# Optimization experiments

Hardware: AMD Instinct MI355X
Metric: run time of the kernel (lower is better)

## Reference

```python
import jax, jax.numpy as jnp
import numpy as np
from jax import lax

ALPHA = 0.1
B, C_IN, T, D_MODEL = 32, 512, 2048, 1024


def setup_inputs() -> dict:
    key = jax.random.key(0)
    k_x, k_w, k_b = jax.random.split(key, 3)
    x = jax.random.normal(k_x, (B, C_IN, T), dtype=jnp.float32)
    # nn.Linear(c_in, d_model): weight [d_model, c_in], bias [d_model]
    bound = 1.0 / np.sqrt(C_IN)
    W = jax.random.uniform(k_w, (D_MODEL, C_IN), dtype=jnp.float32, minval=-bound, maxval=bound)
    b = jax.random.uniform(k_b, (D_MODEL,), dtype=jnp.float32, minval=-bound, maxval=bound)
    return {"x": x, "W": W, "b": b}


def _ewma_scan(xt):
    # xt: [T, B, C] time-major; f_0 = x_0, f_t = a*x_t + (1-a)*f_{t-1}
    def step(carry, xi):
        carry = ALPHA * xi + (1.0 - ALPHA) * carry
        return carry, carry
    _, ys = lax.scan(step, xt[0], xt[1:])
    return jnp.concatenate([xt[:1], ys], axis=0)  # [T, B, C]


def reference(x, W, b):
    # x: [B, c_in, T] -> permute to [B, T, c_in]
    xp = jnp.transpose(x, (0, 2, 1))
    xt = jnp.moveaxis(xp, 1, 0)  # [T, B, c_in]
    fwd = _ewma_scan(xt)
    bwd = _ewma_scan(xt[::-1])[::-1]
    ewma = jnp.moveaxis((fwd + bwd) * 0.5, 0, 1)  # [B, T, c_in]
    # value embedding (dropout = identity at inference)
    return jnp.einsum('btc,dc->btd', ewma, W) + b
```

## Files before the change

kernel.cpp:

```cpp
#include <hip/hip_runtime.h>
#include <hip/hip_bf16.h>
#include <stdint.h>
#include <stddef.h>

#define T_LEN   2048
#define C_IN_   512
#define D_MODEL_ 1024
#define B_SZ    32

typedef __hip_bfloat16 bf16;
typedef __attribute__((ext_vector_type(8))) short short8;
typedef __attribute__((ext_vector_type(4))) float f32x4;

__device__ __forceinline__ void gload16(const void* g, void* l) {
    __builtin_amdgcn_global_load_lds(
        (const __attribute__((address_space(1))) uint32_t*)g,
        (__attribute__((address_space(3))) uint32_t*)l, 16, 0, 0);
}

__global__ void wconv_kernel(const float* __restrict__ W, bf16* __restrict__ Wb) {
    int i = blockIdx.x * 256 + threadIdx.x;
    float4 v = ((const float4*)W)[i];
    bf16* o = Wb + (size_t)i * 4;
    o[0] = __float2bfloat16(v.x);
    o[1] = __float2bfloat16(v.y);
    o[2] = __float2bfloat16(v.z);
    o[3] = __float2bfloat16(v.w);
}

__global__ __launch_bounds__(512)
void ewma_kernel(const float* __restrict__ x, bf16* __restrict__ A) {
    const int tid  = threadIdx.x;
    const int wid  = tid >> 6;
    const int lane = tid & 63;
    const int half = lane >> 5;
    const int j    = lane & 31;
    const int b    = blockIdx.x >> 5;
    const int cg   = blockIdx.x & 31;
    const int c_local = (wid << 1) | half;

    const float AL = 0.1f, OM = 0.9f;
    const float Q  = 1.179018457773862e-3f;

    __shared__ float buf[8 * 2048];
    __shared__ bf16  stg[32 * 16 * 16];

    float xr[64];
    const size_t xbase = ((size_t)b * C_IN_ + (cg << 4)) * T_LEN;
    const int srcu = tid ^ ((tid >> 4) & 7);

    #pragma unroll
    for (int h = 0; h < 2; ++h) {
        #pragma unroll
        for (int it = 0; it < 8; ++it)
            gload16(x + xbase + (size_t)(h * 8 + it) * T_LEN + srcu * 4,
                    (char*)buf + it * 8192 + tid * 16);
        asm volatile("s_waitcnt vmcnt(0)" ::: "memory");
        __syncthreads();
        if ((c_local >> 3) == h) {
            const char* rbase = (const char*)buf + (c_local & 7) * 8192;
            #pragma unroll
            for (int i = 0; i < 16; ++i) {
                int p = (j * 16 + i) ^ (j & 7);
                float4 v = *(const float4*)(rbase + p * 16);
                xr[4*i+0] = v.x; xr[4*i+1] = v.y;
                xr[4*i+2] = v.z; xr[4*i+3] = v.w;
            }
        }
        __syncthreads();
    }

    float g = (j == 0) ? xr[0] : AL * xr[0];
    #pragma unroll
    for (int i = 1; i < 64; ++i) g = fmaf(OM, g, AL * xr[i]);

    float F = g, coef = Q;
    #pragma unroll
    for (int d = 1; d < 32; d <<= 1) {
        float up = __shfl_up(F, d, 32);
        F += (j >= d) ? coef * up : 0.0f;
        coef *= coef;
    }
    float carry = __shfl_up(F, 1, 32);
    if (j == 0) carry = 0.0f;

    xr[0] = (j == 0) ? xr[0] : fmaf(OM, carry, AL * xr[0]);
    #pragma unroll
    for (int i = 1; i < 64; ++i) xr[i] = fmaf(OM, xr[i-1], AL * xr[i]);

    float h2;
    {
        float incL = xr[63] - OM * xr[62];
        if (j == 31) incL *= 10.0f;
        h2 = incL;
        #pragma unroll
        for (int i = 62; i >= 1; --i) h2 = fmaf(OM, h2, xr[i] - OM * xr[i-1]);
        float inc0 = (j == 0) ? AL * xr[0] : (xr[0] - OM * carry);
        h2 = fmaf(OM, h2, inc0);
    }

    float Bv = h2; coef = Q;
    #pragma unroll
    for (int d = 1; d < 32; d <<= 1) {
        float dn = __shfl_down(Bv, d, 32);
        Bv += (j < 32 - d) ? coef * dn : 0.0f;
        coef *= coef;
    }
    float bnext = __shfl_down(Bv, 1, 32);
    if (j == 31) bnext = 0.0f;

    {
        float bp = bnext;
        float incL = xr[63] - OM * xr[62];
        if (j == 31) incL *= 10.0f;
        float bb = fmaf(OM, bp, incL);
        xr[63] = 0.5f * (xr[63] + bb);
        bp = bb;
        #pragma unroll
        for (int i = 62; i >= 1; --i) {
            float inc = xr[i] - OM * xr[i-1];
            bb = fmaf(OM, bp, inc);
            xr[i] = 0.5f * (xr[i] + bb);
            bp = bb;
        }
        float inc0 = (j == 0) ? AL * xr[0] : (xr[0] - OM * carry);
        bb = fmaf(OM, bp, inc0);
        xr[0] = 0.5f * (xr[0] + bb);
    }

    const size_t outbase = (size_t)(b * T_LEN) * C_IN_ + (cg << 4);
    #pragma unroll
    for (int grp = 0; grp < 4; ++grp) {
        __syncthreads();
        #pragma unroll
        for (int ii = 0; ii < 16; ++ii) {
            int elem = ((j * 16 + ii) * 16 + c_local) ^ ((j & 7) << 3);
            stg[elem] = __float2bfloat16(xr[grp * 16 + ii]);
        }
        __syncthreads();
        #pragma unroll
        for (int r = 0; r < 2; ++r) {
            int u   = tid * 2 + r;
            int jj  = u >> 5;
            int ii  = (u >> 1) & 15;
            int hf  = u & 1;
            int elem = ((jj * 16 + ii) * 16 + hf * 8) ^ ((jj & 7) << 3);
            float4 v = *(const float4*)&stg[elem];
            int t = jj * 64 + grp * 16 + ii;
            *(float4*)(A + outbase + (size_t)t * C_IN_ + hf * 8) = v;
        }
    }
}

#define MFMA(a, b, c) __builtin_amdgcn_mfma_f32_16x16x32_bf16(a, b, c, 0, 0, 0)

__global__ __launch_bounds__(256, 2)
void gemm_kernel(const bf16* __restrict__ Amat, const bf16* __restrict__ Wb,
                 const float* __restrict__ bias, float* __restrict__ out) {
    constexpr int K = C_IN_, N = D_MODEL_;
    extern __shared__ bf16 lds[];
    const int tid  = threadIdx.x;
    const int w    = tid >> 6, lane = tid & 63;
    const int lr   = lane & 15;
    const int lg   = lane >> 4;

    int bid = blockIdx.x;
    int swz = (bid & 7) * 256 + (bid >> 3);
    const int mb = swz >> 3, nb = swz & 7;
    const int m0 = mb * 256, n0 = nb * 128;

    auto Abase = [&](int s) -> bf16* { return lds + s * 12288; };
    auto Bbase = [&](int s) -> bf16* { return lds + s * 12288 + 8192; };

    auto stage = [&](int kt, int s) {
        bf16* la = Abase(s);
        #pragma unroll
        for (int r = 0; r < 4; ++r) {
            int q = tid + r * 256;
            int row = q >> 2, u = q & 3;
            gload16(Amat + (size_t)(m0 + row) * K + kt * 32 + ((u ^ ((row >> 1) & 3)) << 3),
                    (char*)la + q * 16);
        }
        bf16* lb = Bbase(s);
        #pragma unroll
        for (int r = 0; r < 2; ++r) {
            int q = tid + r * 256;
            int row = q >> 2, u = q & 3;
            gload16(Wb + (size_t)(n0 + row) * K + kt * 32 + ((u ^ ((row >> 1) & 3)) << 3),
                    (char*)lb + q * 16);
        }
    };
    auto rdA = [&](int s, int f) -> short8 {
        int row = w * 64 + f * 16 + lr;
        return *(const short8*)((const char*)Abase(s)
                                + row * 64 + ((lg ^ ((row >> 1) & 3)) << 4));
    };
    auto rdB = [&](int s, int n) -> short8 {
        int row = n * 16 + lr;
        return *(const short8*)((const char*)Bbase(s)
                                + row * 64 + ((lg ^ ((row >> 1) & 3)) << 4));
    };

    f32x4 acc[4][8];
    #pragma unroll
    for (int f = 0; f < 4; ++f)
        #pragma unroll
        for (int n = 0; n < 8; ++n) acc[f][n] = (f32x4){0.f, 0.f, 0.f, 0.f};

    stage(0, 0);
    stage(1, 1);
    asm volatile("s_waitcnt vmcnt(6)" ::: "memory");
    __builtin_amdgcn_s_barrier();

    #pragma unroll
    for (int kt = 0; kt < 16; ++kt) {
        const int s = kt & 1;
        short8 a[4], b[8];
        #pragma unroll
        for (int f = 0; f < 4; ++f) a[f] = rdA(s, f);
        #pragma unroll
        for (int n = 0; n < 8; ++n) b[n] = rdB(s, n);
        asm volatile("s_waitcnt lgkmcnt(0)");
        __builtin_amdgcn_sched_barrier(0);
        __builtin_amdgcn_s_barrier();

        if (kt < 14) stage(kt + 2, s);

        __builtin_amdgcn_s_setprio(1);
        #pragma unroll
        for (int f = 0; f < 4; ++f)
            #pragma unroll
            for (int n = 0; n < 8; ++n)
                acc[f][n] = MFMA(a[f], b[n], acc[f][n]);
        __builtin_amdgcn_s_setprio(0);

        if (kt < 14)       asm volatile("s_waitcnt vmcnt(6)" ::: "memory");
        else if (kt == 14) asm volatile("s_waitcnt vmcnt(0)" ::: "memory");
        __builtin_amdgcn_s_barrier();
    }

    const int crow = (lane >> 4) << 2;
    #pragma unroll
    for (int n = 0; n < 8; ++n) {
        int col = n0 + n * 16 + lr;
        float bv = bias[col];
        #pragma unroll
        for (int f = 0; f < 4; ++f) {
            size_t rbase = (size_t)(m0 + w * 64 + f * 16 + crow) * N + col;
            #pragma unroll
            for (int r = 0; r < 4; ++r)
                out[rbase + (size_t)r * N] = acc[f][n][r] + bv;
        }
    }
}

extern "C" void kernel_launch(void* const* d_in, const int* in_sizes, int n_in,
                              void* d_out, int out_size, void* d_ws, size_t ws_size,
                              hipStream_t stream) {
    const float* x    = (const float*)d_in[0];
    const float* W    = (const float*)d_in[1];
    const float* bias = (const float*)d_in[2];
    float* out = (float*)d_out;

    bf16* Wb   = (bf16*)d_ws;
    bf16* Amat = (bf16*)((char*)d_ws + (1 << 21));

    hipLaunchKernelGGL(wconv_kernel, dim3(512), dim3(256), 0, stream, W, Wb);
    hipLaunchKernelGGL(ewma_kernel, dim3(B_SZ * 32), dim3(512), 0, stream, x, Amat);
    hipLaunchKernelGGL(gemm_kernel,
                       dim3((B_SZ * T_LEN / 256) * (D_MODEL_ / 128)),
                       dim3(256), 49152, stream, Amat, Wb, bias, out);
}
```

Before: 170.3 us.

## Keep full-K weight tile resident in LDS and stream A directly from global

The GEMM now uses 256x64 output tiles. Each block preloads its entire 64xK slice of the bf16 weight into LDS once, with an XOR swizzle. The A operand is read straight from global memory into registers each k-step instead of through double-buffered LDS staging. This removes the per-iteration barriers and staging, but halves the tile width, doubles the grid and the re-reads of A, and leaves global-load latency for A exposed without explicit prefetch. Block scheduling is also remapped per XCD.

```diff
diff --git a/kernel.cpp b/kernel.cpp
--- a/kernel.cpp
+++ b/kernel.cpp
@@ -159,97 +159,65 @@
                  const float* __restrict__ bias, float* __restrict__ out) {
     constexpr int K = C_IN_, N = D_MODEL_;
     extern __shared__ bf16 lds[];
-    const int tid  = threadIdx.x;
-    const int w    = tid >> 6, lane = tid & 63;
-    const int lr   = lane & 15;
-    const int lg   = lane >> 4;
+    const int tid = threadIdx.x;
+    const int w   = tid >> 6, lane = tid & 63;
+    const int lr  = lane & 15, lg = lane >> 4;
 
     int bid = blockIdx.x;
-    int swz = (bid & 7) * 256 + (bid >> 3);
-    const int mb = swz >> 3, nb = swz & 7;
-    const int m0 = mb * 256, n0 = nb * 128;
-
-    auto Abase = [&](int s) -> bf16* { return lds + s * 12288; };
-    auto Bbase = [&](int s) -> bf16* { return lds + s * 12288 + 8192; };
-
-    auto stage = [&](int kt, int s) {
-        bf16* la = Abase(s);
-        #pragma unroll
-        for (int r = 0; r < 4; ++r) {
-            int q = tid + r * 256;
-            int row = q >> 2, u = q & 3;
-            gload16(Amat + (size_t)(m0 + row) * K + kt * 32 + ((u ^ ((row >> 1) & 3)) << 3),
-                    (char*)la + q * 16);
-        }
-        bf16* lb = Bbase(s);
-        #pragma unroll
-        for (int r = 0; r < 2; ++r) {
-            int q = tid + r * 256;
-            int row = q >> 2, u = q & 3;
-            gload16(Wb + (size_t)(n0 + row) * K + kt * 32 + ((u ^ ((row >> 1) & 3)) << 3),
-                    (char*)lb + q * 16);
-        }
-    };
-    auto rdA = [&](int s, int f) -> short8 {
-        int row = w * 64 + f * 16 + lr;
-        return *(const short8*)((const char*)Abase(s)
-                                + row * 64 + ((lg ^ ((row >> 1) & 3)) << 4));
-    };
-    auto rdB = [&](int s, int n) -> short8 {
-        int row = n * 16 + lr;
-        return *(const short8*)((const char*)Bbase(s)
-                                + row * 64 + ((lg ^ ((row >> 1) & 3)) << 4));
-    };
-
-    f32x4 acc[4][8];
+    int xcd = bid & 7, idx = bid >> 3;
+    int mb  = xcd * 32 + (idx >> 4);
+    int nb  = idx & 15;
+    const int m0 = mb * 256, n0 = nb * 64;
+
+    #pragma unroll
+    for (int r = 0; r < 16; ++r) {
+        int q = tid + r * 256;
+        int row = q >> 6, u = q & 63;
+        gload16(Wb + (size_t)(n0 + row) * K + ((u ^ (row & 7)) << 3),
+                (char*)lds + q * 16);
+    }
+    asm volatile("s_waitcnt vmcnt(0)" ::: "memory");
+    __syncthreads();
+
+    f32x4 acc[4][4];
     #pragma unroll
     for (int f = 0; f < 4; ++f)
         #pragma unroll
-        for (int n = 0; n < 8; ++n) acc[f][n] = (f32x4){0.f, 0.f, 0.f, 0.f};
-
-    stage(0, 0);
-    stage(1, 1);
-    asm volatile("s_waitcnt vmcnt(6)" ::: "memory");
-    __builtin_amdgcn_s_barrier();
+        for (int n = 0; n < 4; ++n) acc[f][n] = (f32x4){0.f, 0.f, 0.f, 0.f};
+
+    const bf16* Ab = Amat + (size_t)(m0 + w * 64) * K;
 
     #pragma unroll
     for (int kt = 0; kt < 16; ++kt) {
-        const int s = kt & 1;
-        short8 a[4], b[8];
-        #pragma unroll
-        for (int f = 0; f < 4; ++f) a[f] = rdA(s, f);
-        #pragma unroll
-        for (int n = 0; n < 8; ++n) b[n] = rdB(s, n);
-        asm volatile("s_waitcnt lgkmcnt(0)");
-        __builtin_amdgcn_sched_barrier(0);
-        __builtin_amdgcn_s_barrier();
-
-        if (kt < 14) stage(kt + 2, s);
-
-        __builtin_amdgcn_s_setprio(1);
+        short8 b[4], a[4];
+        #pragma unroll
+        for (int nf = 0; nf < 4; ++nf) {
+            int row = nf * 16 + lr;
+            b[nf] = *(const short8*)((const char*)lds + row * 1024
+                                     + (((kt * 4 + lg) ^ (row & 7)) << 4));
+        }
+        #pragma unroll
+        for (int f = 0; f < 4; ++f)
+            a[f] = *(const short8*)(Ab + (size_t)(f * 16 + lr) * K
+                                    + kt * 32 + lg * 8);
         #pragma unroll
         for (int f = 0; f < 4; ++f)
             #pragma unroll
-            for (int n = 0; n < 8; ++n)
-                acc[f][n] = MFMA(a[f], b[n], acc[f][n]);
-        __builtin_amdgcn_s_setprio(0);
-
-        if (kt < 14)       asm volatile("s_waitcnt vmcnt(6)" ::: "memory");
-        else if (kt == 14) asm volatile("s_waitcnt vmcnt(0)" ::: "memory");
-        __builtin_amdgcn_s_barrier();
-    }
-
-    const int crow = (lane >> 4) << 2;
-    #pragma unroll
-    for (int n = 0; n < 8; ++n) {
-        int col = n0 + n * 16 + lr;
+            for (int nf = 0; nf < 4; ++nf)
+                acc[f][nf] = MFMA(a[f], b[nf], acc[f][nf]);
+    }
+
+    const int crow = lg << 2;
+    #pragma unroll
+    for (int nf = 0; nf < 4; ++nf) {
+        int col = n0 + nf * 16 + lr;
         float bv = bias[col];
         #pragma unroll
         for (int f = 0; f < 4; ++f) {
             size_t rbase = (size_t)(m0 + w * 64 + f * 16 + crow) * N + col;
             #pragma unroll
             for (int r = 0; r < 4; ++r)
-                out[rbase + (size_t)r * N] = acc[f][n][r] + bv;
+                out[rbase + (size_t)r * N] = acc[f][nf][r] + bv;
         }
     }
 }
@@ -268,6 +236,6 @@
     hipLaunchKernelGGL(wconv_kernel, dim3(512), dim3(256), 0, stream, W, Wb);
     hipLaunchKernelGGL(ewma_kernel, dim3(B_SZ * 32), dim3(512), 0, stream, x, Amat);
     hipLaunchKernelGGL(gemm_kernel,
-                       dim3((B_SZ * T_LEN / 256) * (D_MODEL_ / 128)),
-                       dim3(256), 49152, stream, Amat, Wb, bias, out);
-}
+                       dim3((B_SZ * T_LEN / 256) * (D_MODEL_ / 64)),
+                       dim3(256), 65536, stream, Amat, Wb, bias, out);
+}
```

New measurement: 241.8 us. 42.0% more time.

## Stage GEMM tiles through registers and raise occupancy to three blocks

Applied to the files above, without the earlier changes.

The GEMM prefetch no longer uses direct global-to-LDS loads. Each thread now loads the next K tile into registers, then writes it into the alternate LDS buffer with the XOR swizzle after reading the current fragments. This removes one barrier per iteration and allows a launch bound of three blocks per CU. The extra staging registers plus the tighter register budget from the higher occupancy target could cause spills or VGPR pressure. The global loads also lose their direct LDS path.

```diff
diff --git a/kernel.cpp b/kernel.cpp
--- a/kernel.cpp
+++ b/kernel.cpp
@@ -154,7 +154,7 @@
 
 #define MFMA(a, b, c) __builtin_amdgcn_mfma_f32_16x16x32_bf16(a, b, c, 0, 0, 0)
 
-__global__ __launch_bounds__(256, 2)
+__global__ __launch_bounds__(256, 3)
 void gemm_kernel(const bf16* __restrict__ Amat, const bf16* __restrict__ Wb,
                  const float* __restrict__ bias, float* __restrict__ out) {
     constexpr int K = C_IN_, N = D_MODEL_;
@@ -172,22 +172,29 @@
     auto Abase = [&](int s) -> bf16* { return lds + s * 12288; };
     auto Bbase = [&](int s) -> bf16* { return lds + s * 12288 + 8192; };
 
-    auto stage = [&](int kt, int s) {
-        bf16* la = Abase(s);
-        #pragma unroll
-        for (int r = 0; r < 4; ++r) {
-            int q = tid + r * 256;
-            int row = q >> 2, u = q & 3;
-            gload16(Amat + (size_t)(m0 + row) * K + kt * 32 + ((u ^ ((row >> 1) & 3)) << 3),
-                    (char*)la + q * 16);
-        }
-        bf16* lb = Bbase(s);
-        #pragma unroll
-        for (int r = 0; r < 2; ++r) {
-            int q = tid + r * 256;
-            int row = q >> 2, u = q & 3;
-            gload16(Wb + (size_t)(n0 + row) * K + kt * 32 + ((u ^ ((row >> 1) & 3)) << 3),
-                    (char*)lb + q * 16);
+    auto gld = [&](int kt, short8 r[6]) {
+        #pragma unroll
+        for (int i = 0; i < 4; ++i) {
+            int q = tid + i * 256, row = q >> 2, u = q & 3;
+            r[i] = *(const short8*)(Amat + (size_t)(m0 + row) * K + kt * 32 + u * 8);
+        }
+        #pragma unroll
+        for (int i = 0; i < 2; ++i) {
+            int q = tid + i * 256, row = q >> 2, u = q & 3;
+            r[4 + i] = *(const short8*)(Wb + (size_t)(n0 + row) * K + kt * 32 + u * 8);
+        }
+    };
+    auto sst = [&](int s, short8 r[6]) {
+        bf16* la = Abase(s); bf16* lb = Bbase(s);
+        #pragma unroll
+        for (int i = 0; i < 4; ++i) {
+            int q = tid + i * 256, row = q >> 2, u = q & 3;
+            *(short8*)((char*)la + row * 64 + ((u ^ ((row >> 1) & 3)) << 4)) = r[i];
+        }
+        #pragma unroll
+        for (int i = 0; i < 2; ++i) {
+            int q = tid + i * 256, row = q >> 2, u = q & 3;
+            *(short8*)((char*)lb + row * 64 + ((u ^ ((row >> 1) & 3)) << 4)) = r[4 + i];
         }
     };
     auto rdA = [&](int s, int f) -> short8 {
@@ -207,9 +214,12 @@
         #pragma unroll
         for (int n = 0; n < 8; ++n) acc[f][n] = (f32x4){0.f, 0.f, 0.f, 0.f};
 
-    stage(0, 0);
-    stage(1, 1);
-    asm volatile("s_waitcnt vmcnt(6)" ::: "memory");
+    short8 r[6];
+    gld(0, r);
+    asm volatile("s_waitcnt vmcnt(0)" ::: "memory");
+    sst(0, r);
+    gld(1, r);
+    asm volatile("s_waitcnt lgkmcnt(0)");
     __builtin_amdgcn_s_barrier();
 
     #pragma unroll
@@ -220,11 +230,13 @@
         for (int f = 0; f < 4; ++f) a[f] = rdA(s, f);
         #pragma unroll
         for (int n = 0; n < 8; ++n) b[n] = rdB(s, n);
+        if (kt < 15) {
+            asm volatile("s_waitcnt vmcnt(0)" ::: "memory");
+            sst(s ^ 1, r);
+        }
         asm volatile("s_waitcnt lgkmcnt(0)");
         __builtin_amdgcn_sched_barrier(0);
-        __builtin_amdgcn_s_barrier();
-
-        if (kt < 14) stage(kt + 2, s);
+        if (kt < 14) gld(kt + 2, r);
 
         __builtin_amdgcn_s_setprio(1);
         #pragma unroll
@@ -233,13 +245,10 @@
             for (int n = 0; n < 8; ++n)
                 acc[f][n] = MFMA(a[f], b[n], acc[f][n]);
         __builtin_amdgcn_s_setprio(0);
-
-        if (kt < 14)       asm volatile("s_waitcnt vmcnt(6)" ::: "memory");
-        else if (kt == 14) asm volatile("s_waitcnt vmcnt(0)" ::: "memory");
         __builtin_amdgcn_s_barrier();
     }
 
-    const int crow = (lane >> 4) << 2;
+    const int crow = lg << 2;
     #pragma unroll
     for (int n = 0; n < 8; ++n) {
         int col = n0 + n * 16 + lr;
@@ -248,8 +257,8 @@
         for (int f = 0; f < 4; ++f) {
             size_t rbase = (size_t)(m0 + w * 64 + f * 16 + crow) * N + col;
             #pragma unroll
-            for (int r = 0; r < 4; ++r)
-                out[rbase + (size_t)r * N] = acc[f][n][r] + bv;
+            for (int rr = 0; rr < 4; ++rr)
+                out[rbase + (size_t)rr * N] = acc[f][n][rr] + bv;
         }
     }
 }
```

After: 643.4 us. 3.78x slower.
